# Optimization experiments

Measured on AMD Instinct MI355X. Metric: run time of the kernel, lower is better.

The kernel has to match this reference:

```python
import jax, jax.numpy as jnp
import numpy as np

DEPTH = 8
T = 2 ** (DEPTH + 1) - 1          # 511 tree nodes, parent-pointer array
TREE = np.array([-1] + [(i - 1) // 2 for i in range(1, T)])
BATCH = 32768


def _build_levels(tree):
    # Faithful replication of asym_tree_gen.seq_adj_mat / path_lengths /
    # find_all_leaf_ids, producing per-level (rows, cols) of the sparse masks.
    n = len(tree)
    in_tree = set(int(v) for v in tree)
    leaves = [i for i in range(n) if i not in in_tree]
    L = len(leaves)
    leaf_set = set(leaves)
    paths = np.zeros(n, dtype=np.int64)
    for s in range(n):
        node, p = s, 0
        branch = node
        while branch != 0:
            branch = tree[node]
            node = branch
            p += 1
        paths[s] = p
    i = j = 1
    ids = np.arange(n)
    levels = []
    for path_len in reversed(range(int(paths.max()) + 1)):
        nodes = ids[paths == path_len]
        rows, cols = [], []
        for nd in nodes:          # leaf nodes first (matches original loop order)
            if nd in leaf_set:
                rows.append(nd); cols.append(L - i); i += 1
        for nd in nodes:          # then branch nodes
            if nd not in leaf_set:
                rows += [nd, nd]
                cols += [n + L - j, n + L - j - 1]
                j += 2
        levels.append((np.array(rows, dtype=np.int32), np.array(cols, dtype=np.int32)))
    return levels, L


LEVELS, L = _build_levels(TREE)
NLEV = len(LEVELS)  # 9 levels for a depth-8 full binary tree


def _nck(z, alpha, beta, gamma):
    # NCK activation (scale=1): alpha*f_Na + beta*f_Ca + gamma*f_K
    f_na = 0.0878 * (z - 113.68) / (1.0 + jnp.exp(6.39 - z / 8.98))
    f_ca = 0.129 * (z - 69.62) / (1.0 + jnp.exp(-4.4 - z / 4.25))
    f_k = 2.23 / (0.436 + jnp.exp(-0.132 * (z - 16.74)))
    return alpha * f_na + beta * f_ca + gamma * f_k


def _forward(x, ws, bs, alpha, beta, gamma, root_w, root_b):
    B = x.shape[0]
    hidden = jnp.concatenate([x, jnp.zeros((B, T), x.dtype)], axis=1)  # [B, L+T]
    for l in range(NLEV):
        rows, cols = LEVELS[l]
        contrib = hidden[:, cols] * ws[l][None, :]                     # [B, nnz_l]
        z = jax.ops.segment_sum(contrib.T, rows, num_segments=T).T     # [B, T]
        z = z + bs[l][None, :]
        hidden = jnp.concatenate([x, _nck(z, alpha, beta, gamma)], axis=1)
    y = hidden[:, L:L + 1]                   # root node (tree node 0) output
    out = y @ root_w.T + root_b              # root: Linear(Repeats=1, 1)
    return jax.nn.sigmoid(out)


def setup_inputs():
    key = jax.random.key(0)
    ks = jax.random.split(key, NLEV + 3)
    inp = {"x": jax.random.normal(ks[0], (BATCH, L), dtype=jnp.float32)}
    for l in range(NLEV):
        nnz = LEVELS[l][0].shape[0]
        inp[f"w{l}"] = jax.random.normal(ks[l + 1], (nnz,), dtype=jnp.float32) * 0.5
        inp[f"b{l}"] = jnp.zeros((T,), dtype=jnp.float32)   # bias.data.zero_()
    inp["alpha"] = jnp.array([1.0], dtype=jnp.float32)
    inp["beta"] = jnp.array([0.6], dtype=jnp.float32)
    inp["gamma"] = jnp.array([1.0], dtype=jnp.float32)
    inp["root_w"] = jax.random.normal(ks[NLEV + 1], (1, 1), dtype=jnp.float32)
    inp["root_b"] = jnp.zeros((1,), dtype=jnp.float32)
    return inp


def reference(x, w0, w1, w2, w3, w4, w5, w6, w7, w8,
              b0, b1, b2, b3, b4, b5, b6, b7, b8,
              alpha, beta, gamma, root_w, root_b):
    ws = [w0, w1, w2, w3, w4, w5, w6, w7, w8]
    bs = [b0, b1, b2, b3, b4, b5, b6, b7, b8]
    return _forward(x, ws, bs, alpha, beta, gamma, root_w, root_b)
```

## Files before the change

kernel.cpp:

```cpp
#include <hip/hip_runtime.h>

#ifndef __has_builtin
#define __has_builtin(x) 0
#endif

#if __has_builtin(__builtin_amdgcn_exp2f)
#define EXP2F(x) __builtin_amdgcn_exp2f(x)
#else
#define EXP2F(x) exp2f(x)
#endif

#if __has_builtin(__builtin_amdgcn_rcpf)
#define RCPF(x) __builtin_amdgcn_rcpf(x)
#else
#define RCPF(x) (1.0f / (x))
#endif

#define LOG2E_F 1.4426950408889634f

#define CA1 (-0.16065646437f)
#define CA0 ( 9.2188213109f)
#define CB1 (-0.33945766845f)
#define CB0 (-6.3478581799f)
#define CC1 (-0.19043574540f)
#define CC0 ( 3.1878943779f)

struct TreeParams {
  const float* w[9];
  const float* b[9];
};

__device__ __forceinline__ float nck_eval(float z, float A1, float A0,
                                          float B1, float B0, float G) {
  float ea = EXP2F(fmaf(z, CA1, CA0));
  float eb = EXP2F(fmaf(z, CB1, CB0));
  float ec = EXP2F(fmaf(z, CC1, CC0));
  float ra = RCPF(1.0f + ea);
  float rb = RCPF(1.0f + eb);
  float rc = RCPF(0.436f + ec);
  return fmaf(fmaf(z, A1, A0), ra, fmaf(fmaf(z, B1, B0), rb, G * rc));
}


__global__ __launch_bounds__(256, 2)
void asym_tree_fwd(const float* __restrict__ x, TreeParams p,
                   const float* __restrict__ alpha_p,
                   const float* __restrict__ beta_p,
                   const float* __restrict__ gamma_p,
                   const float* __restrict__ rw_p,
                   const float* __restrict__ rb_p,
                   float* __restrict__ out) {
  __shared__ float xs[64 * 257];
  __shared__ float wc[766];
  __shared__ float bc[511];
  __shared__ float stk[7 * 256];
  __shared__ float v2[4][64];

  const int tid = threadIdx.x;

  {
    const int wsz[9] = {256, 256, 128, 64, 32, 16, 8, 4, 2};
    int off = 0;
#pragma unroll
    for (int l = 0; l < 9; ++l) {
      if (tid < wsz[l]) wc[off + tid] = p.w[l][tid];
      off += wsz[l];
    }
#pragma unroll
    for (int l = 0; l < 9; ++l) {
      int d = 8 - l;
      int base = (1 << d) - 1;
      int cnt = 1 << d;
      for (int i = tid; i < cnt; i += 256) bc[base + i] = p.b[l][base + i];
    }
  }

  {
    const float4* src =
        reinterpret_cast<const float4*>(x + (size_t)blockIdx.x * 64 * 256);
#pragma unroll
    for (int it = 0; it < 16; ++it) {
      int f4 = it * 256 + tid;
      float4 v = src[f4];
      int e = f4 >> 6;
      int c = (f4 & 63) << 2;
      float* dst = &xs[e * 257 + c];
      dst[0] = v.x; dst[1] = v.y; dst[2] = v.z; dst[3] = v.w;
    }
  }
  __syncthreads();

  const float alpha = alpha_p[0], beta = beta_p[0], gamma = gamma_p[0];
  const float A1 = alpha * 0.0878f, A0 = -A1 * 113.68f;
  const float B1 = beta * 0.129f,   B0 = -B1 * 69.62f;
  const float G  = gamma * 2.23f;

  const int e = tid & 63;
  const int j = tid >> 6;
  const float* xrow = &xs[e * 257];

  float v = 0.0f;
#pragma unroll 4
  for (int t = 0; t < 64; ++t) {
    const int ig = (j << 6) | t;
    const int k8 = ig ^ 0x55;
    const int col = ig ^ 0xAA;
    v = nck_eval(fmaf(xrow[col], wc[k8], bc[255 + k8]), A1, A0, B1, B0, G);

    int dv = 8;
    int tt = t;
    while (tt & 1) {
      const float vl = stk[(dv - 2) * 256 + tid];
      dv -= 1;
      const int kd = (ig >> (8 - dv)) ^ (0x55 & ((1 << dv) - 1));
      const int wo = 768 - (1 << (dv + 2));
      const float z = fmaf(wc[wo + 2 * kd], vl,
                           fmaf(wc[wo + 2 * kd + 1], v,
                                bc[(1 << dv) - 1 + kd]));
      v = nck_eval(z, A1, A0, B1, B0, G);
      tt >>= 1;
    }
    stk[(dv - 2) * 256 + tid] = v;
  }
  v2[j][e] = v;
  __syncthreads();

  if (tid < 64) {
    const float vA = nck_eval(
        fmaf(wc[762], v2[0][tid], fmaf(wc[763], v2[1][tid], bc[2])),
        A1, A0, B1, B0, G);
    const float vB = nck_eval(
        fmaf(wc[760], v2[2][tid], fmaf(wc[761], v2[3][tid], bc[1])),
        A1, A0, B1, B0, G);
    const float y = nck_eval(fmaf(wc[764], vA, fmaf(wc[765], vB, bc[0])),
                             A1, A0, B1, B0, G);
    const float o = fmaf(rw_p[0], y, rb_p[0]);
    out[(size_t)blockIdx.x * 64 + tid] =
        RCPF(1.0f + EXP2F(-o * LOG2E_F));
  }
}

extern "C" void kernel_launch(void* const* d_in, const int* in_sizes, int n_in,
                              void* d_out, int out_size, void* d_ws,
                              size_t ws_size, hipStream_t stream) {
  (void)n_in; (void)d_ws; (void)ws_size; (void)out_size;
  const float* x = (const float*)d_in[0];
  TreeParams p;
  for (int l = 0; l < 9; ++l) {
    p.w[l] = (const float*)d_in[1 + 2 * l];
    p.b[l] = (const float*)d_in[2 + 2 * l];
  }
  const float* alpha = (const float*)d_in[19];
  const float* beta  = (const float*)d_in[20];
  const float* gamma = (const float*)d_in[21];
  const float* rw    = (const float*)d_in[22];
  const float* rb    = (const float*)d_in[23];
  float* out = (float*)d_out;

  const int batch = in_sizes[0] / 256;
  const int grid = batch / 64;
  asym_tree_fwd<<<grid, 256, 0, stream>>>(x, p, alpha, beta, gamma, rw, rb, out);
}
```

Before: 145.0 us.

## Evaluate tree subtrees in registers via compile-time recursion with 8 warps per sample

Replaces the shared-memory staging of x and the runtime stack-based post-order traversal with a template-recursive subtree evaluator. Each thread now loads its 32 leaf inputs straight into registers as float4s. The block grows to 512 threads so eight waves each handle one depth-3 subtree per sample, and the final three levels are reduced by the first wave. This removes the large xs shared buffer and the stack traffic, which should raise occupancy and remove LDS round trips. The costs are higher register pressure from the fully unrolled tree, uncoalesced per-row global loads of 128 bytes per thread, and more serial work left to one wave at the end.

```diff
diff --git a/kernel.cpp b/kernel.cpp
--- a/kernel.cpp
+++ b/kernel.cpp
@@ -42,7 +42,44 @@
 }
 
 
-__global__ __launch_bounds__(256, 2)
+template <int I>
+__device__ __forceinline__ float xget(const float4* xr) {
+  constexpr int q = I >> 2, r = I & 3;
+  if constexpr (r == 0) return xr[q].x;
+  else if constexpr (r == 1) return xr[q].y;
+  else if constexpr (r == 2) return xr[q].z;
+  else return xr[q].w;
+}
+
+struct Ctx {
+  const float4* xr;
+  const float* wc;
+  const float* bc;
+  int w;
+  float A1, A0, B1, B0, G;
+};
+
+template <int D, int CPRE>
+__device__ __forceinline__ float node_eval(const Ctx& c) {
+  if constexpr (D == 8) {
+    constexpr int t = CPRE;
+    const int k8 = ((c.w ^ 2) << 5) | (t ^ 0x15);
+    const float xv = xget<(t ^ 0x0A)>(c.xr);
+    return nck_eval(fmaf(xv, c.wc[k8], c.bc[255 + k8]),
+                    c.A1, c.A0, c.B1, c.B0, c.G);
+  } else {
+    const float a = node_eval<D + 1, 2 * CPRE>(c);
+    const float b = node_eval<D + 1, 2 * CPRE + 1>(c);
+    const int k = ((c.w << (D - 3)) | CPRE) ^ (0x55 & ((1 << D) - 1));
+    constexpr int wo = 768 - (1 << (D + 2));
+    const float z = fmaf(c.wc[wo + 2 * k], a,
+                         fmaf(c.wc[wo + 2 * k + 1], b,
+                              c.bc[(1 << D) - 1 + k]));
+    return nck_eval(z, c.A1, c.A0, c.B1, c.B0, c.G);
+  }
+}
+
+__global__ __launch_bounds__(512, 4)
 void asym_tree_fwd(const float* __restrict__ x, TreeParams p,
                    const float* __restrict__ alpha_p,
                    const float* __restrict__ beta_p,
@@ -50,13 +87,19 @@
                    const float* __restrict__ rw_p,
                    const float* __restrict__ rb_p,
                    float* __restrict__ out) {
-  __shared__ float xs[64 * 257];
   __shared__ float wc[766];
   __shared__ float bc[511];
-  __shared__ float stk[7 * 256];
-  __shared__ float v2[4][64];
+  __shared__ float v3[8][64];
 
   const int tid = threadIdx.x;
+  const int e = tid & 63;
+  const int w = tid >> 6;
+
+  const float4* xsrc = reinterpret_cast<const float4*>(
+      x + (((size_t)blockIdx.x * 64 + e) * 256 + ((w ^ 5) << 5)));
+  float4 xr[8];
+#pragma unroll
+  for (int i = 0; i < 8; ++i) xr[i] = xsrc[i];
 
   {
     const int wsz[9] = {256, 256, 128, 64, 32, 16, 8, 4, 2};
@@ -71,72 +114,43 @@
       int d = 8 - l;
       int base = (1 << d) - 1;
       int cnt = 1 << d;
-      for (int i = tid; i < cnt; i += 256) bc[base + i] = p.b[l][base + i];
-    }
-  }
-
-  {
-    const float4* src =
-        reinterpret_cast<const float4*>(x + (size_t)blockIdx.x * 64 * 256);
-#pragma unroll
-    for (int it = 0; it < 16; ++it) {
-      int f4 = it * 256 + tid;
-      float4 v = src[f4];
-      int e = f4 >> 6;
-      int c = (f4 & 63) << 2;
-      float* dst = &xs[e * 257 + c];
-      dst[0] = v.x; dst[1] = v.y; dst[2] = v.z; dst[3] = v.w;
+      for (int i = tid; i < cnt; i += 512) bc[base + i] = p.b[l][base + i];
     }
   }
   __syncthreads();
 
   const float alpha = alpha_p[0], beta = beta_p[0], gamma = gamma_p[0];
-  const float A1 = alpha * 0.0878f, A0 = -A1 * 113.68f;
-  const float B1 = beta * 0.129f,   B0 = -B1 * 69.62f;
-  const float G  = gamma * 2.23f;
+  Ctx c;
+  c.xr = xr; c.wc = wc; c.bc = bc; c.w = w;
+  c.A1 = alpha * 0.0878f; c.A0 = -c.A1 * 113.68f;
+  c.B1 = beta * 0.129f;   c.B0 = -c.B1 * 69.62f;
+  c.G  = gamma * 2.23f;
 
-  const int e = tid & 63;
-  const int j = tid >> 6;
-  const float* xrow = &xs[e * 257];
-
-  float v = 0.0f;
-#pragma unroll 4
-  for (int t = 0; t < 64; ++t) {
-    const int ig = (j << 6) | t;
-    const int k8 = ig ^ 0x55;
-    const int col = ig ^ 0xAA;
-    v = nck_eval(fmaf(xrow[col], wc[k8], bc[255 + k8]), A1, A0, B1, B0, G);
-
-    int dv = 8;
-    int tt = t;
-    while (tt & 1) {
-      const float vl = stk[(dv - 2) * 256 + tid];
-      dv -= 1;
-      const int kd = (ig >> (8 - dv)) ^ (0x55 & ((1 << dv) - 1));
-      const int wo = 768 - (1 << (dv + 2));
-      const float z = fmaf(wc[wo + 2 * kd], vl,
-                           fmaf(wc[wo + 2 * kd + 1], v,
-                                bc[(1 << dv) - 1 + kd]));
-      v = nck_eval(z, A1, A0, B1, B0, G);
-      tt >>= 1;
-    }
-    stk[(dv - 2) * 256 + tid] = v;
-  }
-  v2[j][e] = v;
+  v3[w][e] = node_eval<3, 0>(c);
   __syncthreads();
 
-  if (tid < 64) {
-    const float vA = nck_eval(
-        fmaf(wc[762], v2[0][tid], fmaf(wc[763], v2[1][tid], bc[2])),
-        A1, A0, B1, B0, G);
-    const float vB = nck_eval(
-        fmaf(wc[760], v2[2][tid], fmaf(wc[761], v2[3][tid], bc[1])),
-        A1, A0, B1, B0, G);
-    const float y = nck_eval(fmaf(wc[764], vA, fmaf(wc[765], vB, bc[0])),
-                             A1, A0, B1, B0, G);
+  if (w == 0) {
+    float v2[4];
+#pragma unroll
+    for (int q = 0; q < 4; ++q) {
+      const int k2 = q ^ 1;
+      v2[q] = nck_eval(fmaf(wc[752 + 2 * k2], v3[2 * q][e],
+                            fmaf(wc[753 + 2 * k2], v3[2 * q + 1][e],
+                                 bc[3 + k2])),
+                       c.A1, c.A0, c.B1, c.B0, c.G);
+    }
+    float v1[2];
+#pragma unroll
+    for (int q = 0; q < 2; ++q) {
+      const int k1 = q ^ 1;
+      v1[q] = nck_eval(fmaf(wc[760 + 2 * k1], v2[2 * q],
+                            fmaf(wc[761 + 2 * k1], v2[2 * q + 1], bc[1 + k1])),
+                       c.A1, c.A0, c.B1, c.B0, c.G);
+    }
+    const float y = nck_eval(fmaf(wc[764], v1[0], fmaf(wc[765], v1[1], bc[0])),
+                             c.A1, c.A0, c.B1, c.B0, c.G);
     const float o = fmaf(rw_p[0], y, rb_p[0]);
-    out[(size_t)blockIdx.x * 64 + tid] =
-        RCPF(1.0f + EXP2F(-o * LOG2E_F));
+    out[(size_t)blockIdx.x * 64 + e] = RCPF(1.0f + EXP2F(-o * LOG2E_F));
   }
 }
 
@@ -159,5 +173,6 @@
 
   const int batch = in_sizes[0] / 256;
   const int grid = batch / 64;
-  asym_tree_fwd<<<grid, 256, 0, stream>>>(x, p, alpha, beta, gamma, rw, rb, out);
+  asym_tree_fwd<<<grid, 512, 0, stream>>>(x, p, alpha, beta, gamma, rw, rb,
+                                          out);
 }
```

Result: faster. 140.0 us, median of 2 (-3.4%).
